# Kernel optimization log

Hardware: AMD Instinct MI355X
Metric: run time of the kernel (lower is better)

The kernel has to match this reference:

```python
import jax, jax.numpy as jnp
import numpy as np
from jax import lax

B, C, H, W = 2, 64, 48, 48
NH, DK, DV = 8, 64, 128          # heads, per-head d_k, per-head d_v
DN, NS, R = 128, 16, 4           # SS2D d_inner (expand=2), d_state, dt_rank
MULT = 4                          # FFN expansion
L = H * W


def layer_norm(x, w, b, eps=1e-5):
    m = x.mean(-1, keepdims=True)
    v = ((x - m) ** 2).mean(-1, keepdims=True)
    return (x - m) / jnp.sqrt(v + eps) * w + b


def conv2d(x, w, groups=1):
    # x: NCHW, w: OIHW
    return lax.conv_general_dilated(x, w, (1, 1), 'SAME',
                                    dimension_numbers=('NCHW', 'OIHW', 'NCHW'),
                                    feature_group_count=groups)


def setup_inputs() -> dict:
    key = jax.random.key(0)
    ks = jax.random.split(key, 24)
    rn = lambda k, shp, s=0.02: jax.random.normal(k, shp, jnp.float32) * s
    inp = {
        'enc_input': jax.random.normal(ks[0], (B, C, H, W), jnp.float32),
        'slf_attn_snr': jax.random.uniform(ks[1], (B, 1, H, W), jnp.float32),
        # MultiHeadAttention params
        'attn_wq': rn(ks[2], (C, NH * DK)),
        'attn_wk': rn(ks[3], (C, NH * DK)),
        'attn_wv': rn(ks[4], (C, NH * DV)),
        'attn_fc': rn(ks[5], (NH * DV, C)),
        'attn_ln_w': jnp.ones((C,), jnp.float32),
        'attn_ln_b': jnp.zeros((C,), jnp.float32),
        # SS2D params
        'ss_in_w': rn(ks[6], (C, 2 * DN)),
        'ss_conv_w': rn(ks[7], (DN, 1, 3, 3)),
        'ss_conv_b': jnp.zeros((DN,), jnp.float32),
        'ss_xproj_w': rn(ks[8], (4, R + 2 * NS, DN)),
        'ss_dt_w': rn(ks[9], (4, DN, R)),
        'ss_dt_b': rn(ks[10], (4, DN)),
        'ss_Alog': jnp.log(jnp.broadcast_to(jnp.arange(1, NS + 1, dtype=jnp.float32), (4, DN, NS))),
        'ss_D': jnp.ones((4, DN), jnp.float32),
        'ss_norm_w': jnp.ones((DN,), jnp.float32),
        'ss_norm_b': jnp.zeros((DN,), jnp.float32),
        'ss_out_w': rn(ks[11], (DN, C)),
        # FFN (PreNorm + conv block)
        'ffn_ln_w': jnp.ones((C,), jnp.float32),
        'ffn_ln_b': jnp.zeros((C,), jnp.float32),
        'ffn_w1': rn(ks[12], (C * MULT, C, 1, 1)),
        'ffn_dw': rn(ks[13], (C * MULT, 1, 3, 3)),
        'ffn_w2': rn(ks[14], (C, C * MULT, 1, 1)),
    }
    return inp


def reference(enc_input, slf_attn_snr, attn_wq, attn_wk, attn_wv, attn_fc,
              attn_ln_w, attn_ln_b, ss_in_w, ss_conv_w, ss_conv_b, ss_xproj_w,
              ss_dt_w, ss_dt_b, ss_Alog, ss_D, ss_norm_w, ss_norm_b, ss_out_w,
              ffn_ln_w, ffn_ln_b, ffn_w1, ffn_dw, ffn_w2):
    # ---- Multi-head self-attention over spatial tokens (SNR-biased) ----
    x_tok = enc_input.reshape(B, C, L).transpose(0, 2, 1)        # (B, L, C)
    q = (x_tok @ attn_wq).reshape(B, L, NH, DK).transpose(0, 2, 1, 3)
    k = (x_tok @ attn_wk).reshape(B, L, NH, DK).transpose(0, 2, 1, 3)
    v = (x_tok @ attn_wv).reshape(B, L, NH, DV).transpose(0, 2, 1, 3)
    scores = jnp.einsum('bhqd,bhkd->bhqk', q, k) / jnp.sqrt(jnp.float32(DK))
    snr_flat = slf_attn_snr.reshape(B, 1, 1, L)                  # bias over keys
    scores = scores + jnp.log(snr_flat + 1e-4)
    attn = jax.nn.softmax(scores, axis=-1)                       # (B, NH, L, L)
    o = jnp.einsum('bhqk,bhkd->bhqd', attn, v)
    o = o.transpose(0, 2, 1, 3).reshape(B, L, NH * DV) @ attn_fc
    enc_output = layer_norm(o + x_tok, attn_ln_w, attn_ln_b)     # post-LN residual
    enc_output = enc_output.transpose(0, 2, 1).reshape(B, C, H, W)

    # ---- SS2D: 4-direction 2D selective scan ----
    xh = enc_output.transpose(0, 2, 3, 1)                        # (B, H, W, C)
    snr_h = slf_attn_snr.transpose(0, 2, 3, 1)                   # (B, H, W, 1)
    xz = xh @ ss_in_w                                            # (B, H, W, 2*DN)
    x1, z = xz[..., :DN], xz[..., DN:]
    x1 = x1.transpose(0, 3, 1, 2)                                # (B, DN, H, W)
    x1 = conv2d(x1, ss_conv_w, groups=DN) + ss_conv_b[None, :, None, None]
    x1 = jax.nn.silu(x1)

    x_hw = x1.reshape(B, DN, L)
    x_wh = x1.transpose(0, 1, 3, 2).reshape(B, DN, L)
    xs = jnp.stack([x_hw, x_wh], axis=1)                         # (B, 2, DN, L)
    xs = jnp.concatenate([xs, jnp.flip(xs, axis=-1)], axis=1)    # (B, 4, DN, L)

    x_dbl = jnp.einsum('bkdl,kcd->bkcl', xs, ss_xproj_w)
    dts, Bs, Cs = x_dbl[:, :, :R], x_dbl[:, :, R:R + NS], x_dbl[:, :, R + NS:]
    dts = jnp.einsum('bkrl,kdr->bkdl', dts, ss_dt_w) + ss_dt_b[None, :, :, None]
    dts = jax.nn.softplus(dts)                                   # (B, 4, DN, L)
    A = -jnp.exp(ss_Alog)                                        # (4, DN, NS)

    def step(h, inp):
        xt, dtt, Bt, Ct = inp                                    # (B,4,DN),(B,4,DN),(B,4,NS),(B,4,NS)
        dA = jnp.exp(dtt[..., None] * A)                         # (B,4,DN,NS)
        h = h * dA + (dtt * xt)[..., None] * Bt[:, :, None, :]
        y = jnp.einsum('bkdn,bkn->bkd', h, Ct)
        return h, y

    h0 = jnp.zeros((B, 4, DN, NS), jnp.float32)
    elems = (xs.transpose(3, 0, 1, 2), dts.transpose(3, 0, 1, 2),
             Bs.transpose(3, 0, 1, 2), Cs.transpose(3, 0, 1, 2))
    _, ys = lax.scan(step, h0, elems)                            # (L, B, 4, DN)
    ys = ys.transpose(1, 2, 3, 0) + ss_D[None, :, :, None] * xs  # (B, 4, DN, L)

    inv = jnp.flip(ys[:, 2:4], axis=-1)                          # undo reversed scans
    wh = ys[:, 1].reshape(B, DN, W, H).transpose(0, 1, 3, 2).reshape(B, DN, L)
    invwh = inv[:, 1].reshape(B, DN, W, H).transpose(0, 1, 3, 2).reshape(B, DN, L)
    y = ys[:, 0] + inv[:, 0] + wh + invwh                        # (B, DN, L)
    y = y.transpose(0, 2, 1).reshape(B, H, W, DN)
    y = layer_norm(y, ss_norm_w, ss_norm_b) * jax.nn.silu(z) * snr_h
    x2 = y @ ss_out_w + enc_input.transpose(0, 2, 3, 1)          # (B, H, W, C)

    # ---- PreNorm conv FeedForward ----
    xn = layer_norm(x2, ffn_ln_w, ffn_ln_b).transpose(0, 3, 1, 2)
    h1 = jax.nn.gelu(conv2d(xn, ffn_w1), approximate=False)
    h1 = jax.nn.gelu(conv2d(h1, ffn_dw, groups=C * MULT), approximate=False)
    h1 = conv2d(h1, ffn_w2).transpose(0, 2, 3, 1)
    x3 = h1 + x2

    return x3.transpose(0, 3, 1, 2)                              # (B, C, H, W)
```

## Files before the change

### kernel.cpp

```cpp
#include <hip/hip_runtime.h>
#include <hip/hip_bf16.h>

#define Bq 2
#define Cc 64
#define Hh 48
#define Ww 48
#define Ll 2304
#define NHh 8
#define DKk 64
#define DVv 128
#define DNn 128
#define NSs 16
#define Rr 4
#define SCH 48
#define SNC 48
#define TT 8

#define OQ    0u
#define OK_   2359296u
#define OV    4718592u
#define OO    9437184u
#define OLP   14450688u
#define OX2   15040512u
#define OVT   15630336u
#define WS_NEED_FLOATS (OVT + 4718592u)
#define ODT2  OQ
#define OYS2  OK_
#define OX1P  OV
#define OZ    (OV + 589824u)
#define OX1S  (OV + 1179648u)
#define OBS2  (OV + 1769472u)
#define OCS2  (OV + 2064384u)
#define OCSA  (OV + 2359296u)
#define OCSB  (OV + 3145728u)
#define OHST  (OV + 3932160u)
#define OH1A  OO
#define OH1B  (OO + 1179648u)

typedef short short8v __attribute__((ext_vector_type(8)));
typedef short short4v __attribute__((ext_vector_type(4)));
typedef float f32x4 __attribute__((ext_vector_type(4)));
typedef unsigned short ushort_t;

__device__ __forceinline__ float geluf(float x) {
  return 0.5f * x * (1.0f + erff(x * 0.70710678118654752f));
}
__device__ __forceinline__ float siluf(float x) {
  return x / (1.0f + __expf(-x));
}
__device__ __forceinline__ float softplusf(float x) {
  return fmaxf(x, 0.0f) + log1pf(__expf(-fabsf(x)));
}
__device__ __forceinline__ int spmap(int k, int l) {
  if (k == 0) return l;
  if (k == 1) return (l % 48) * 48 + l / 48;
  if (k == 2) return 2303 - l;
  int l2 = 2303 - l; return (l2 % 48) * 48 + l2 / 48;
}
__device__ __forceinline__ short f2bf(float f) {
  unsigned u = __float_as_uint(f);
  unsigned r = (u + 0x7FFFu + ((u >> 16) & 1u)) >> 16;
  return (short)r;
}

__global__ void k_code(float* out) { if (threadIdx.x == 0) out[0] = 25000.f; }

__global__ __launch_bounds__(256) void k_qkv(const float* __restrict__ enc,
    const float* __restrict__ wq, const float* __restrict__ wk,
    const float* __restrict__ wv, float* __restrict__ ws) {
  int l0 = blockIdx.x * TT; int b = blockIdx.y;
  int t = threadIdx.x;
  __shared__ float xs[64][12];
  {
    int idx = t, c = idx >> 3, i = idx & 7;
    xs[c][i] = enc[(size_t)b * Cc * Ll + (size_t)c * Ll + l0 + i];
    idx = t + 256; c = idx >> 3; i = idx & 7;
    xs[c][i] = enc[(size_t)b * Cc * Ll + (size_t)c * Ll + l0 + i];
  }
  __syncthreads();
  ushort_t* qb = (ushort_t*)(ws + OQ);
  ushort_t* kb = (ushort_t*)(ws + OK_);
  float* v = ws + OV;
#pragma unroll
  for (int g = 0; g < 6; ++g) {
    int j = t + g * 256;
    float acc[TT];
#pragma unroll
    for (int i = 0; i < TT; ++i) acc[i] = 0.f;
    const float* wp; int col, stride;
    if (j < 512) { wp = wq + j; stride = 512; col = j; }
    else if (j < 1024) { wp = wk + (j - 512); stride = 512; col = j - 512; }
    else { wp = wv + (j - 1024); stride = 1024; col = j - 1024; }
    for (int c = 0; c < 64; ++c) {
      float w = wp[(size_t)c * stride];
      const float4* xc = (const float4*)&xs[c][0];
      float4 x0 = xc[0], x1 = xc[1];
      acc[0] += x0.x * w; acc[1] += x0.y * w;
      acc[2] += x0.z * w; acc[3] += x0.w * w;
      acc[4] += x1.x * w; acc[5] += x1.y * w;
      acc[6] += x1.z * w; acc[7] += x1.w * w;
    }
    if (j < 512) {
#pragma unroll
      for (int i = 0; i < TT; ++i)
        qb[((size_t)(b * 8 + (col >> 6)) * Ll + l0 + i) * 64 + (col & 63)] =
            (ushort_t)f2bf(acc[i] * 0.125f);
    } else if (j < 1024) {
#pragma unroll
      for (int i = 0; i < TT; ++i)
        kb[((size_t)(b * 8 + (col >> 6)) * Ll + l0 + i) * 64 + (col & 63)] =
            (ushort_t)f2bf(acc[i]);
    } else {
#pragma unroll
      for (int i = 0; i < TT; ++i)
        v[((size_t)(b * 8 + (col >> 7)) * Ll + l0 + i) * 128 + (col & 127)] = acc[i];
    }
  }
}

__global__ __launch_bounds__(256) void k_vt(float* __restrict__ ws) {
  int bh = blockIdx.y;
  int l0 = blockIdx.x * 64;
  int t = threadIdx.x;
  __shared__ float tile[128][65];
  const float* vp = ws + OV + ((size_t)bh * Ll + l0) * 128;
  for (int i = t; i < 64 * 32; i += 256) {
    int l = i >> 5, dv4 = (i & 31) * 4;
    float4 a = *(const float4*)(vp + (size_t)l * 128 + dv4);
    tile[dv4][l] = a.x; tile[dv4 + 1][l] = a.y;
    tile[dv4 + 2][l] = a.z; tile[dv4 + 3][l] = a.w;
  }
  __syncthreads();
  ushort_t* vt = (ushort_t*)(ws + OVT) + (size_t)bh * 128 * Ll + l0;
  for (int i = t; i < 128 * 16; i += 256) {
    int dv = i >> 4, l4 = (i & 15) * 4;
    short4v a;
    a[0] = f2bf(tile[dv][l4]); a[1] = f2bf(tile[dv][l4 + 1]);
    a[2] = f2bf(tile[dv][l4 + 2]); a[3] = f2bf(tile[dv][l4 + 3]);
    *(short4v*)(vt + (size_t)dv * Ll + l4) = a;
  }
}

#define NKT2 18
#define LSK 72
__global__ __launch_bounds__(256) void k_attn(const float* __restrict__ snr,
                                              float* __restrict__ ws) {
  int bh = blockIdx.y; int b = bh >> 3; int hd = bh & 7;
  int q0 = blockIdx.x * 64;
  int ks = blockIdx.z;
  int kbase = ks * (Ll / 2);
  int t = threadIdx.x;
  int w = t >> 6, lane = t & 63;
  int m16 = lane & 15, quad = lane >> 4;

  __shared__ __align__(16) ushort_t Ks[64 * LSK];
  __shared__ __align__(16) ushort_t Vs[128 * LSK];
  __shared__ __align__(16) ushort_t Ps[4 * 16 * LSK];
  __shared__ float sfac_s[64];

  const ushort_t* qbf = (const ushort_t*)(ws + OQ) + (size_t)bh * Ll * 64;
  const ushort_t* kbf = (const ushort_t*)(ws + OK_) + (size_t)bh * Ll * 64;
  const ushort_t* vtb = (const ushort_t*)(ws + OVT) + (size_t)bh * 128 * Ll;

  short8v qa[2];
  {
    const ushort_t* qrp = qbf + (size_t)(q0 + w * 16 + m16) * 64 + quad * 8;
    qa[0] = *(const short8v*)qrp;
    qa[1] = *(const short8v*)(qrp + 32);
  }
  int sk_key = t >> 2, sk_d0 = (t & 3) * 16;
  int sv_dv = t >> 1, sv_k0 = (t & 1) * 32;

  short8v kreg[2], vreg[4];
  float snr_reg = 0.f;
  {
    const ushort_t* ksrc = kbf + (size_t)(kbase + sk_key) * 64 + sk_d0;
    kreg[0] = *(const short8v*)ksrc;
    kreg[1] = *(const short8v*)(ksrc + 8);
    const ushort_t* vsrc = vtb + (size_t)sv_dv * Ll + kbase + sv_k0;
#pragma unroll
    for (int i = 0; i < 4; ++i) vreg[i] = *(const short8v*)(vsrc + i * 8);
    if (t < 64) snr_reg = snr[b * Ll + kbase + t];
  }

  f32x4 oacc[8];
#pragma unroll
  for (int i = 0; i < 8; ++i) oacc[i] = (f32x4)0.f;
  float l_r[4] = {0.f, 0.f, 0.f, 0.f};

  for (int kt = 0; kt < NKT2; ++kt) {
    __syncthreads();
    *(short8v*)&Ks[sk_key * LSK + sk_d0] = kreg[0];
    *(short8v*)&Ks[sk_key * LSK + sk_d0 + 8] = kreg[1];
#pragma unroll
    for (int i = 0; i < 4; ++i)
      *(short8v*)&Vs[sv_dv * LSK + sv_k0 + i * 8] = vreg[i];
    if (t < 64) sfac_s[t] = snr_reg + 1e-4f;
    __syncthreads();
    if (kt + 1 < NKT2) {
      int k0n = kbase + (kt + 1) * 64;
      const ushort_t* ksrc = kbf + (size_t)(k0n + sk_key) * 64 + sk_d0;
      kreg[0] = *(const short8v*)ksrc;
      kreg[1] = *(const short8v*)(ksrc + 8);
      const ushort_t* vsrc = vtb + (size_t)sv_dv * Ll + k0n + sv_k0;
#pragma unroll
      for (int i = 0; i < 4; ++i) vreg[i] = *(const short8v*)(vsrc + i * 8);
      if (t < 64) snr_reg = snr[b * Ll + k0n + t];
    }

    f32x4 sac[4];
#pragma unroll
    for (int n = 0; n < 4; ++n) {
      int key = n * 16 + m16;
      short8v kb0 = *(const short8v*)&Ks[key * LSK + quad * 8];
      short8v kb1 = *(const short8v*)&Ks[key * LSK + 32 + quad * 8];
      f32x4 acc = (f32x4)0.f;
      acc = __builtin_amdgcn_mfma_f32_16x16x32_bf16(qa[0], kb0, acc, 0, 0, 0);
      acc = __builtin_amdgcn_mfma_f32_16x16x32_bf16(qa[1], kb1, acc, 0, 0, 0);
      sac[n] = acc;
    }
    float sf[4];
#pragma unroll
    for (int n = 0; n < 4; ++n) sf[n] = sfac_s[n * 16 + m16];
    ushort_t* pw = &Ps[w * 16 * LSK];
#pragma unroll
    for (int r = 0; r < 4; ++r) {
#pragma unroll
      for (int n = 0; n < 4; ++n) {
        float p = __expf(sac[n][r]) * sf[n];
        l_r[r] += p;
        pw[(quad * 4 + r) * LSK + n * 16 + m16] = (ushort_t)f2bf(p);
      }
    }
    short8v pb0 = *(const short8v*)&pw[m16 * LSK + quad * 8];
    short8v pb1 = *(const short8v*)&pw[m16 * LSK + 32 + quad * 8];
#pragma unroll
    for (int dt_ = 0; dt_ < 8; ++dt_) {
      const ushort_t* vrow = &Vs[(dt_ * 16 + m16) * LSK];
      short8v va0 = *(const short8v*)&vrow[quad * 8];
      short8v va1 = *(const short8v*)&vrow[32 + quad * 8];
      f32x4 o = oacc[dt_];
      o = __builtin_amdgcn_mfma_f32_16x16x32_bf16(va0, pb0, o, 0, 0, 0);
      o = __builtin_amdgcn_mfma_f32_16x16x32_bf16(va1, pb1, o, 0, 0, 0);
      oacc[dt_] = o;
    }
  }
#pragma unroll
  for (int r = 0; r < 4; ++r) {
    float lv = l_r[r];
    lv += __shfl_xor(lv, 1, 64);
    lv += __shfl_xor(lv, 2, 64);
    lv += __shfl_xor(lv, 4, 64);
    lv += __shfl_xor(lv, 8, 64);
    l_r[r] = lv;
  }
  if (m16 == 0) {
    float* lp = ws + OLP + (size_t)ks * (Bq * NHh * Ll) + (size_t)bh * Ll;
#pragma unroll
    for (int r = 0; r < 4; ++r) lp[q0 + w * 16 + quad * 4 + r] = l_r[r];
  }
  float* opb = ws + (ks ? OV : OO);
  float* op = opb + ((size_t)(b * Ll + q0 + w * 16 + m16)) * 1024 + hd * 128;
#pragma unroll
  for (int dt_ = 0; dt_ < 8; ++dt_) {
#pragma unroll
    for (int r = 0; r < 4; ++r) {
      op[dt_ * 16 + quad * 4 + r] = oacc[dt_][r];
    }
  }
}

__global__ __launch_bounds__(256) void k_ocomb(float* __restrict__ ws) {
  size_t e4 = (size_t)blockIdx.x * 256 + threadIdx.x;
  int c4 = (int)(e4 & 255);
  size_t bl = e4 >> 8;
  int b = (int)(bl / Ll), l = (int)(bl % Ll);
  int hd = c4 >> 5;
  int bh = b * 8 + hd;
  float l1 = ws[OLP + (size_t)bh * Ll + l];
  float l2 = ws[OLP + (size_t)(Bq * NHh * Ll) + (size_t)bh * Ll + l];
  float linv = 1.f / (l1 + l2);
  float4* po = (float4*)(ws + OO) + e4;
  const float4* pv = (const float4*)(ws + OV) + e4;
  float4 a = *po, bq = *pv;
  a.x = (a.x + bq.x) * linv;
  a.y = (a.y + bq.y) * linv;
  a.z = (a.z + bq.z) * linv;
  a.w = (a.w + bq.w) * linv;
  *po = a;
}

__global__ __launch_bounds__(256) void k_oprojxz(const float* __restrict__ enc,
    const float* __restrict__ fc, const float* __restrict__ lnw,
    const float* __restrict__ lnb, const float* __restrict__ ssin,
    float* __restrict__ ws) {
  int l0 = blockIdx.x * TT, b = blockIdx.y, t = threadIdx.x;
  __shared__ float orow[1024][9];
  __shared__ float part[4][TT][64];
  __shared__ float xh_s[64][9];
  const float* op = ws + OO + ((size_t)(b * Ll + l0)) * 1024;
#pragma unroll
  for (int k = 0; k < 4; ++k) {
    int c = t + k * 256;
#pragma unroll
    for (int i = 0; i < TT; ++i) orow[c][i] = op[(size_t)i * 1024 + c];
  }
  __syncthreads();
  int col = t & 63, seg = t >> 6;
  {
    float acc[TT];
#pragma unroll
    for (int i = 0; i < TT; ++i) acc[i] = 0.f;
    const float* fcs = fc + (size_t)(seg * 256) * 64 + col;
    for (int c = 0; c < 256; ++c) {
      float w = fcs[(size_t)c * 64];
      const float* orc = &orow[seg * 256 + c][0];
#pragma unroll
      for (int i = 0; i < TT; ++i) acc[i] += orc[i] * w;
    }
#pragma unroll
    for (int i = 0; i < TT; ++i) part[seg][i][col] = acc[i];
  }
  __syncthreads();
  if (t < 64) {
    float lw = lnw[t], lb = lnb[t];
#pragma unroll
    for (int i = 0; i < TT; ++i) {
      float a = part[0][i][t] + part[1][i][t] + part[2][i][t] + part[3][i][t];
      a += enc[(size_t)b * Cc * Ll + (size_t)t * Ll + l0 + i];
      float s = a;
#pragma unroll
      for (int o = 32; o >= 1; o >>= 1) s += __shfl_xor(s, o, 64);
      float m = s * (1.f / 64.f);
      float dd = a - m;
      float vs = dd * dd;
#pragma unroll
      for (int o = 32; o >= 1; o >>= 1) vs += __shfl_xor(vs, o, 64);
      xh_s[t][i] = dd * rsqrtf(vs * (1.f / 64.f) + 1e-5f) * lw + lb;
    }
  }
  __syncthreads();
  {
    float acc2[TT];
#pragma unroll
    for (int i = 0; i < TT; ++i) acc2[i] = 0.f;
    for (int c = 0; c < 64; ++c) {
      float w = ssin[c * 256 + t];
      const float* xc = &xh_s[c][0];
#pragma unroll
      for (int i = 0; i < TT; ++i) acc2[i] += xc[i] * w;
    }
    if (t < 128) {
#pragma unroll
      for (int i = 0; i < TT; ++i)
        ws[OX1P + ((size_t)(b * Ll + l0 + i)) * 128 + t] = acc2[i];
    } else {
#pragma unroll
      for (int i = 0; i < TT; ++i)
        ws[OZ + ((size_t)(b * Ll + l0 + i)) * 128 + (t - 128)] = acc2[i];
    }
  }
}

__global__ __launch_bounds__(256) void k_conv(const float* __restrict__ cw,
    const float* __restrict__ cb, float* __restrict__ ws) {
  int l0 = blockIdx.x * TT, b = blockIdx.y, t = threadIdx.x;
  int h = l0 / 48, w0 = l0 % 48;
  __shared__ float tile[3][10][128];
  for (int idx = t; idx < 3840; idx += 256) {
    int r = idx / 1280, rem = idx % 1280;
    int col = rem >> 7, d = rem & 127;
    int hh = h + r - 1, wx = w0 + col - 1;
    float v = 0.f;
    if (hh >= 0 && hh < 48 && wx >= 0 && wx < 48)
      v = ws[OX1P + ((size_t)(b * Ll + hh * 48 + wx)) * 128 + d];
    tile[r][col][d] = v;
  }
  __syncthreads();
  int d = t & 127, half = t >> 7;
  float cwr[9];
#pragma unroll
  for (int j = 0; j < 9; ++j) cwr[j] = cw[d * 9 + j];
  float cbv = cb[d];
#pragma unroll
  for (int j = 0; j < 4; ++j) {
    int i = half * 4 + j;
    float acc = cbv;
#pragma unroll
    for (int kh = 0; kh < 3; ++kh)
#pragma unroll
      for (int kw = 0; kw < 3; ++kw)
        acc += tile[kh][i + kw][d] * cwr[kh * 3 + kw];
    ws[OX1S + ((size_t)(b * Ll + l0 + i)) * 128 + d] = siluf(acc);
  }
}

__global__ __launch_bounds__(128) void k_xdbl(const float* __restrict__ xw,
    const float* __restrict__ dtw, const float* __restrict__ dtb,
    float* __restrict__ ws) {
  int l0 = blockIdx.x * TT;
  int by = blockIdx.y; int b = by >> 2; int k = by & 3;
  int t = threadIdx.x;
  __shared__ float xv[128][9];
  __shared__ float pr[36][TT];
#pragma unroll
  for (int i = 0; i < TT; ++i) {
    int sp = spmap(k, l0 + i);
    xv[t][i] = ws[OX1S + ((size_t)(b * Ll) + sp) * 128 + t];
  }
  __syncthreads();
  if (t < 36) {
    float s[TT];
#pragma unroll
    for (int i = 0; i < TT; ++i) s[i] = 0.f;
    const float* wp = xw + (size_t)(k * 36 + t) * 128;
    for (int d = 0; d < 128; ++d) {
      float w = wp[d];
      const float* xc = &xv[d][0];
#pragma unroll
      for (int i = 0; i < TT; ++i) s[i] += xc[i] * w;
    }
#pragma unroll
    for (int i = 0; i < TT; ++i) pr[t][i] = s[i];
  }
  __syncthreads();
  {
    int d = t;
    const float* wp = dtw + (size_t)(k * 128 + d) * 4;
    float w0 = wp[0], w1 = wp[1], w2 = wp[2], w3 = wp[3];
    float bb = dtb[k * 128 + d];
#pragma unroll
    for (int i = 0; i < TT; ++i) {
      float v = pr[0][i] * w0 + pr[1][i] * w1 + pr[2][i] * w2 + pr[3][i] * w3 + bb;
      ws[ODT2 + ((size_t)(by * Ll + l0 + i)) * 128 + d] = softplusf(v);
    }
  }
  if (t < 16) {
#pragma unroll
    for (int i = 0; i < TT; ++i)
      ws[OBS2 + ((size_t)(by * Ll + l0 + i)) * 16 + t] = pr[4 + t][i];
  } else if (t < 32) {
#pragma unroll
    for (int i = 0; i < TT; ++i)
      ws[OCS2 + ((size_t)(by * Ll + l0 + i)) * 16 + (t - 16)] = pr[20 + (t - 16)][i];
  }
}

__global__ __launch_bounds__(256) void k_scanA(const float* __restrict__ alog,
                                               float* __restrict__ ws) {
  int c = blockIdx.x;
  int bk = blockIdx.y;
  int b = bk >> 2, k = bk & 3;
  int t = threadIdx.x;
  int n = t & 15, dg = t >> 4;
  __shared__ float dt_s[2][128], x_s[2][128], Bs_s[2][16];
  float A_r[8], ap[8], bc[8];
#pragma unroll
  for (int i = 0; i < 8; ++i) {
    int d = dg * 8 + i;
    A_r[i] = -__expf(alog[(size_t)((k * 128 + d) * 16) + n]);
    ap[i] = 1.f; bc[i] = 0.f;
  }
  const float* dtp = ws + ODT2 + ((size_t)bk * Ll) * 128;
  const float* bsp = ws + OBS2 + ((size_t)bk * Ll) * 16;
  const float* xb = ws + OX1S + (size_t)b * Ll * 128;
  float r_a = 0.f, r_Bs = 0.f;
  {
    int l = c * SCH;
    int sp = spmap(k, l);
    if (t < 128) r_a = dtp[(size_t)l * 128 + t];
    else r_a = xb[(size_t)sp * 128 + (t - 128)];
    if (t < 16) r_Bs = bsp[(size_t)l * 16 + t];
  }
  for (int ll = 0; ll < SCH; ++ll) {
    int buf = ll & 1;
    if (t < 128) dt_s[buf][t] = r_a;
    else x_s[buf][t - 128] = r_a;
    if (t < 16) Bs_s[buf][t] = r_Bs;
    __syncthreads();
    if (ll + 1 < SCH) {
      int l2 = c * SCH + ll + 1;
      int sp2 = spmap(k, l2);
      if (t < 128) r_a = dtp[(size_t)l2 * 128 + t];
      else r_a = xb[(size_t)sp2 * 128 + (t - 128)];
      if (t < 16) r_Bs = bsp[(size_t)l2 * 16 + t];
    }
    float Bv = Bs_s[buf][n];
#pragma unroll
    for (int i = 0; i < 8; ++i) {
      int d = dg * 8 + i;
      float dtv = dt_s[buf][d];
      float a = __expf(dtv * A_r[i]);
      bc[i] = bc[i] * a + dtv * x_s[buf][d] * Bv;
      ap[i] *= a;
    }
  }
  float* csa = ws + OCSA + ((size_t)(bk * SNC + c) * 128) * 16;
  float* csb = ws + OCSB + ((size_t)(bk * SNC + c) * 128) * 16;
#pragma unroll
  for (int i = 0; i < 8; ++i) {
    int d = dg * 8 + i;
    csa[d * 16 + n] = ap[i];
    csb[d * 16 + n] = bc[i];
  }
}

__global__ __launch_bounds__(256) void k_scanB(float* __restrict__ ws) {
  int g = blockIdx.x * 256 + threadIdx.x;
  int bk = g >> 11;
  int dn = g & 2047;
  const float* csa = ws + OCSA;
  const float* csb = ws + OCSB;
  float* hst = ws + OHST;
  size_t base = (size_t)bk * SNC * 2048 + dn;
  float h = 0.f;
  float a = csa[base], bq = csb[base];
  for (int c = 0; c < SNC; ++c) {
    float na = 0.f, nb = 0.f;
    if (c + 1 < SNC) {
      size_t idx2 = base + (size_t)(c + 1) * 2048;
      na = csa[idx2]; nb = csb[idx2];
    }
    hst[base + (size_t)c * 2048] = h;
    h = a * h + bq;
    a = na; bq = nb;
  }
}

__global__ __launch_bounds__(256) void k_scanC(const float* __restrict__ alog,
    const float* __restrict__ Dp, float* __restrict__ ws) {
  int c = blockIdx.x, bk = blockIdx.y;
  int b = bk >> 2, k = bk & 3;
  int t = threadIdx.x;
  int n = t & 15, dg = t >> 4;
  __shared__ float dt_s[2][128], x_s[2][128], Bs_s[2][16], Cs_s[2][16];
  float A_r[8], h[8], Dv[8];
#pragma unroll
  for (int i = 0; i < 8; ++i) {
    int d = dg * 8 + i;
    A_r[i] = -__expf(alog[(size_t)((k * 128 + d) * 16) + n]);
    h[i] = ws[OHST + ((size_t)(bk * SNC + c) * 128 + d) * 16 + n];
    Dv[i] = Dp[k * 128 + d];
  }
  const float* dtp = ws + ODT2 + ((size_t)bk * Ll) * 128;
  const float* bsp = ws + OBS2 + ((size_t)bk * Ll) * 16;
  const float* csp = ws + OCS2 + ((size_t)bk * Ll) * 16;
  const float* xb = ws + OX1S + (size_t)b * Ll * 128;
  float* yp = ws + OYS2 + ((size_t)bk * Ll) * 128;
  float r_a = 0.f, r_bc = 0.f;
  {
    int l = c * SCH;
    int sp = spmap(k, l);
    if (t < 128) r_a = dtp[(size_t)l * 128 + t];
    else r_a = xb[(size_t)sp * 128 + (t - 128)];
    if (t < 16) r_bc = bsp[(size_t)l * 16 + t];
    else if (t < 32) r_bc = csp[(size_t)l * 16 + (t - 16)];
  }
  for (int ll = 0; ll < SCH; ++ll) {
    int buf = ll & 1;
    if (t < 128) dt_s[buf][t] = r_a;
    else x_s[buf][t - 128] = r_a;
    if (t < 16) Bs_s[buf][t] = r_bc;
    else if (t < 32) Cs_s[buf][t - 16] = r_bc;
    __syncthreads();
    if (ll + 1 < SCH) {
      int l2 = c * SCH + ll + 1;
      int sp2 = spmap(k, l2);
      if (t < 128) r_a = dtp[(size_t)l2 * 128 + t];
      else r_a = xb[(size_t)sp2 * 128 + (t - 128)];
      if (t < 16) r_bc = bsp[(size_t)l2 * 16 + t];
      else if (t < 32) r_bc = csp[(size_t)l2 * 16 + (t - 16)];
    }
    int l = c * SCH + ll;
    float Bv = Bs_s[buf][n], Cv = Cs_s[buf][n];
    float yacc[8];
#pragma unroll
    for (int i = 0; i < 8; ++i) {
      int d = dg * 8 + i;
      float dtv = dt_s[buf][d];
      float a = __expf(dtv * A_r[i]);
      h[i] = h[i] * a + dtv * x_s[buf][d] * Bv;
      yacc[i] = h[i] * Cv;
    }
#pragma unroll
    for (int i = 0; i < 8; ++i) {
      float yv = yacc[i];
      yv += __shfl_xor(yv, 1, 64);
      yv += __shfl_xor(yv, 2, 64);
      yv += __shfl_xor(yv, 4, 64);
      yv += __shfl_xor(yv, 8, 64);
      yacc[i] = yv;
    }
    if (n == 0) {
#pragma unroll
      for (int i = 0; i < 8; ++i) {
        int d = dg * 8 + i;
        yp[(size_t)l * 128 + d] = yacc[i] + Dv[i] * x_s[buf][d];
      }
    }
  }
}

__global__ __launch_bounds__(256) void k_combffn1(const float* __restrict__ enc,
    const float* __restrict__ nw, const float* __restrict__ nb,
    const float* __restrict__ snr, const float* __restrict__ ow,
    const float* __restrict__ lw, const float* __restrict__ lb,
    const float* __restrict__ w1, float* __restrict__ ws) {
  int l0 = blockIdx.x * TT, b = blockIdx.y, t = threadIdx.x;
  __shared__ float yr[128][9];
  __shared__ float redm[2][TT], redq[2][TT];
  __shared__ float part[2][TT][64];
  __shared__ float xn_s[64][9];
  int lane = t & 63, wid = (t >> 6) & 1;
  float v[TT], m[TT];
  if (t < 128) {
    int d = t;
    const float* ysb = ws + OYS2;
#pragma unroll
    for (int i = 0; i < TT; ++i) {
      int l = l0 + i;
      int hh = l / 48, wwp = l % 48;
      int lT = wwp * 48 + hh;
      v[i] = ysb[((size_t)(b * 4 + 0) * Ll + l) * 128 + d] +
             ysb[((size_t)(b * 4 + 2) * Ll + (2303 - l)) * 128 + d] +
             ysb[((size_t)(b * 4 + 1) * Ll + lT) * 128 + d] +
             ysb[((size_t)(b * 4 + 3) * Ll + (2303 - lT)) * 128 + d];
    }
    float s[TT];
#pragma unroll
    for (int i = 0; i < TT; ++i) s[i] = v[i];
#pragma unroll
    for (int o = 32; o >= 1; o >>= 1)
#pragma unroll
      for (int i = 0; i < TT; ++i) s[i] += __shfl_xor(s[i], o, 64);
    if (lane == 0) {
#pragma unroll
      for (int i = 0; i < TT; ++i) redm[wid][i] = s[i];
    }
  }
  __syncthreads();
  if (t < 128) {
    float q[TT];
#pragma unroll
    for (int i = 0; i < TT; ++i) {
      m[i] = (redm[0][i] + redm[1][i]) * (1.f / 128.f);
      float dv = v[i] - m[i];
      q[i] = dv * dv;
    }
#pragma unroll
    for (int o = 32; o >= 1; o >>= 1)
#pragma unroll
      for (int i = 0; i < TT; ++i) q[i] += __shfl_xor(q[i], o, 64);
    if (lane == 0) {
#pragma unroll
      for (int i = 0; i < TT; ++i) redq[wid][i] = q[i];
    }
  }
  __syncthreads();
  if (t < 128) {
    int d = t;
    float nwv = nw[d], nbv = nb[d];
#pragma unroll
    for (int i = 0; i < TT; ++i) {
      int l = l0 + i;
      float var = (redq[0][i] + redq[1][i]) * (1.f / 128.f);
      float y = (v[i] - m[i]) * rsqrtf(var + 1e-5f) * nwv + nbv;
      float zv = ws[OZ + ((size_t)(b * Ll + l)) * 128 + d];
      y *= siluf(zv);
      y *= snr[b * Ll + l];
      yr[d][i] = y;
    }
  }
  __syncthreads();
  if (t < 128) {
    int col = t & 63, seg = t >> 6;
    float acc[TT];
#pragma unroll
    for (int i = 0; i < TT; ++i) acc[i] = 0.f;
    const float* ows = ow + (size_t)(seg * 64) * 64 + col;
    for (int c = 0; c < 64; ++c) {
      float w = ows[c * 64];
      const float* yc = &yr[seg * 64 + c][0];
#pragma unroll
      for (int i = 0; i < TT; ++i) acc[i] += yc[i] * w;
    }
#pragma unroll
    for (int i = 0; i < TT; ++i) part[seg][i][col] = acc[i];
  }
  __syncthreads();
  if (t < 64) {
    float lwv = lw[t], lbv = lb[t];
#pragma unroll
    for (int i = 0; i < TT; ++i) {
      float a = part[0][i][t] + part[1][i][t];
      a += enc[(size_t)b * Cc * Ll + (size_t)t * Ll + l0 + i];
      ws[OX2 + ((size_t)(b * Ll + l0 + i)) * 64 + t] = a;
      float s = a;
#pragma unroll
      for (int o = 32; o >= 1; o >>= 1) s += __shfl_xor(s, o, 64);
      float mm = s * (1.f / 64.f);
      float dd2 = a - mm;
      float vs = dd2 * dd2;
#pragma unroll
      for (int o = 32; o >= 1; o >>= 1) vs += __shfl_xor(vs, o, 64);
      xn_s[t][i] = dd2 * rsqrtf(vs * (1.f / 64.f) + 1e-5f) * lwv + lbv;
    }
  }
  __syncthreads();
  {
    float acc2[TT];
#pragma unroll
    for (int i = 0; i < TT; ++i) acc2[i] = 0.f;
    const float* wp = w1 + (size_t)t * 64;
    for (int c = 0; c < 64; ++c) {
      float w = wp[c];
      const float* xc = &xn_s[c][0];
#pragma unroll
      for (int i = 0; i < TT; ++i) acc2[i] += xc[i] * w;
    }
#pragma unroll
    for (int i = 0; i < TT; ++i)
      ws[OH1A + ((size_t)(b * Ll + l0 + i)) * 256 + t] = geluf(acc2[i]);
  }
}

__global__ __launch_bounds__(256) void k_ffndw(const float* __restrict__ dww,
                                               float* __restrict__ ws) {
  int l0 = blockIdx.x * TT, b = blockIdx.y, t = threadIdx.x;
  int h = l0 / 48, w0 = l0 % 48;
  __shared__ float tile[3][10][256];
  for (int idx = t; idx < 7680; idx += 256) {
    int r = idx / 2560, rem = idx % 2560;
    int col = rem >> 8, ch = rem & 255;
    int hh = h + r - 1, wx = w0 + col - 1;
    float v = 0.f;
    if (hh >= 0 && hh < 48 && wx >= 0 && wx < 48)
      v = ws[OH1A + ((size_t)(b * Ll + hh * 48 + wx)) * 256 + ch];
    tile[r][col][ch] = v;
  }
  __syncthreads();
  float dwr[9];
#pragma unroll
  for (int j = 0; j < 9; ++j) dwr[j] = dww[t * 9 + j];
#pragma unroll
  for (int i = 0; i < TT; ++i) {
    float acc = 0.f;
#pragma unroll
    for (int kh = 0; kh < 3; ++kh)
#pragma unroll
      for (int kw = 0; kw < 3; ++kw)
        acc += tile[kh][i + kw][t] * dwr[kh * 3 + kw];
    ws[OH1B + ((size_t)(b * Ll + l0 + i)) * 256 + t] = geluf(acc);
  }
}

__global__ __launch_bounds__(256) void k_ffn2(const float* __restrict__ w2,
                                              float* __restrict__ ws,
                                              float* __restrict__ out) {
  int l0 = blockIdx.x * TT, b = blockIdx.y, t = threadIdx.x;
  __shared__ float hr[256][9];
  __shared__ float part[4][TT][64];
  const float* hp = ws + OH1B + ((size_t)(b * Ll + l0)) * 256;
#pragma unroll
  for (int i = 0; i < TT; ++i) hr[t][i] = hp[(size_t)i * 256 + t];
  __syncthreads();
  int col = t & 63, seg = t >> 6;
  {
    float acc[TT];
#pragma unroll
    for (int i = 0; i < TT; ++i) acc[i] = 0.f;
    const float* wp = w2 + (size_t)col * 256 + seg * 64;
    for (int c = 0; c < 64; ++c) {
      float w = wp[c];
      const float* hc = &hr[seg * 64 + c][0];
#pragma unroll
      for (int i = 0; i < TT; ++i) acc[i] += hc[i] * w;
    }
#pragma unroll
    for (int i = 0; i < TT; ++i) part[seg][i][col] = acc[i];
  }
  __syncthreads();
  if (t < 64) {
    float av[TT];
#pragma unroll
    for (int i = 0; i < TT; ++i) {
      float a = part[0][i][t] + part[1][i][t] + part[2][i][t] + part[3][i][t];
      av[i] = a + ws[OX2 + ((size_t)(b * Ll + l0 + i)) * 64 + t];
    }
    float* opx = out + ((size_t)(b * 64 + t)) * 2304 + l0;
    *(float4*)opx = make_float4(av[0], av[1], av[2], av[3]);
    *((float4*)opx + 1) = make_float4(av[4], av[5], av[6], av[7]);
  }
}

extern "C" void kernel_launch(void* const* d_in, const int* in_sizes, int n_in,
                              void* d_out, int out_size, void* d_ws, size_t ws_size,
                              hipStream_t stream) {
  (void)in_sizes; (void)n_in; (void)out_size;
  const float* enc  = (const float*)d_in[0];
  const float* snr  = (const float*)d_in[1];
  const float* wq   = (const float*)d_in[2];
  const float* wk   = (const float*)d_in[3];
  const float* wv   = (const float*)d_in[4];
  const float* fc   = (const float*)d_in[5];
  const float* alnw = (const float*)d_in[6];
  const float* alnb = (const float*)d_in[7];
  const float* ssin = (const float*)d_in[8];
  const float* cw   = (const float*)d_in[9];
  const float* cb   = (const float*)d_in[10];
  const float* xw   = (const float*)d_in[11];
  const float* dtw  = (const float*)d_in[12];
  const float* dtb  = (const float*)d_in[13];
  const float* alog = (const float*)d_in[14];
  const float* Dp   = (const float*)d_in[15];
  const float* nw   = (const float*)d_in[16];
  const float* nb   = (const float*)d_in[17];
  const float* ow   = (const float*)d_in[18];
  const float* flnw = (const float*)d_in[19];
  const float* flnb = (const float*)d_in[20];
  const float* w1   = (const float*)d_in[21];
  const float* dww  = (const float*)d_in[22];
  const float* w2   = (const float*)d_in[23];
  float* ws = (float*)d_ws;
  float* out = (float*)d_out;

  if (ws_size < (size_t)WS_NEED_FLOATS * 4) {
    hipLaunchKernelGGL(k_code, dim3(1), dim3(64), 0, stream, out);
    return;
  }

  hipLaunchKernelGGL(k_qkv, dim3(Ll / TT, Bq), dim3(256), 0, stream, enc, wq, wk, wv, ws);
  hipLaunchKernelGGL(k_vt, dim3(Ll / 64, Bq * NHh), dim3(256), 0, stream, ws);
  hipLaunchKernelGGL(k_attn, dim3(Ll / 64, Bq * NHh, 2), dim3(256), 0, stream, snr, ws);
  hipLaunchKernelGGL(k_ocomb, dim3(Bq * Ll, 1), dim3(256), 0, stream, ws);
  hipLaunchKernelGGL(k_oprojxz, dim3(Ll / TT, Bq), dim3(256), 0, stream, enc, fc, alnw, alnb, ssin, ws);
  hipLaunchKernelGGL(k_conv, dim3(Ll / TT, Bq), dim3(256), 0, stream, cw, cb, ws);
  hipLaunchKernelGGL(k_xdbl, dim3(Ll / TT, Bq * 4), dim3(128), 0, stream, xw, dtw, dtb, ws);
  hipLaunchKernelGGL(k_scanA, dim3(SNC, Bq * 4), dim3(256), 0, stream, alog, ws);
  hipLaunchKernelGGL(k_scanB, dim3(64), dim3(256), 0, stream, ws);
  hipLaunchKernelGGL(k_scanC, dim3(SNC, Bq * 4), dim3(256), 0, stream, alog, Dp, ws);
  hipLaunchKernelGGL(k_combffn1, dim3(Ll / TT, Bq), dim3(256), 0, stream, enc, nw, nb, snr, ow, flnw, flnb, w1, ws);
  hipLaunchKernelGGL(k_ffndw, dim3(Ll / TT, Bq), dim3(256), 0, stream, dww, ws);
  hipLaunchKernelGGL(k_ffn2, dim3(Ll / TT, Bq), dim3(256), 0, stream, w2, ws, out);
}
```

Measured before the change: 433.7 us.

## Fuse split-K attention output combine into output projection kernel

Removes the separate k_ocomb kernel. k_oprojxz now reads both split-K partial outputs and the two softmax denominators, then combines and normalises them while loading into shared memory. This saves one launch plus a full read-modify-write pass over the 1024-wide attention output. The workspace layout is reshuffled so X1P, Z, LP and X2 no longer alias buffers that are still live. Separately, the LayerNorm stages in two kernels now spread over all four wavefronts instead of only the first 64 threads.

```diff
diff --git a/kernel.cpp b/kernel.cpp
--- a/kernel.cpp
+++ b/kernel.cpp
@@ -20,14 +20,14 @@
 #define OK_   2359296u
 #define OV    4718592u
 #define OO    9437184u
-#define OLP   14450688u
-#define OX2   15040512u
+#define OX1P  14450688u
+#define OZ    15040512u
 #define OVT   15630336u
+#define OLP   (OVT + 2359296u)
+#define OX2   0u
 #define WS_NEED_FLOATS (OVT + 4718592u)
 #define ODT2  OQ
 #define OYS2  OK_
-#define OX1P  OV
-#define OZ    (OV + 589824u)
 #define OX1S  (OV + 1179648u)
 #define OBS2  (OV + 1769472u)
 #define OCS2  (OV + 2064384u)
@@ -270,26 +270,6 @@
   }
 }
 
-__global__ __launch_bounds__(256) void k_ocomb(float* __restrict__ ws) {
-  size_t e4 = (size_t)blockIdx.x * 256 + threadIdx.x;
-  int c4 = (int)(e4 & 255);
-  size_t bl = e4 >> 8;
-  int b = (int)(bl / Ll), l = (int)(bl % Ll);
-  int hd = c4 >> 5;
-  int bh = b * 8 + hd;
-  float l1 = ws[OLP + (size_t)bh * Ll + l];
-  float l2 = ws[OLP + (size_t)(Bq * NHh * Ll) + (size_t)bh * Ll + l];
-  float linv = 1.f / (l1 + l2);
-  float4* po = (float4*)(ws + OO) + e4;
-  const float4* pv = (const float4*)(ws + OV) + e4;
-  float4 a = *po, bq = *pv;
-  a.x = (a.x + bq.x) * linv;
-  a.y = (a.y + bq.y) * linv;
-  a.z = (a.z + bq.z) * linv;
-  a.w = (a.w + bq.w) * linv;
-  *po = a;
-}
-
 __global__ __launch_bounds__(256) void k_oprojxz(const float* __restrict__ enc,
     const float* __restrict__ fc, const float* __restrict__ lnw,
     const float* __restrict__ lnb, const float* __restrict__ ssin,
@@ -298,12 +278,25 @@
   __shared__ float orow[1024][9];
   __shared__ float part[4][TT][64];
   __shared__ float xh_s[64][9];
-  const float* op = ws + OO + ((size_t)(b * Ll + l0)) * 1024;
+  __shared__ float linv_s[8][TT];
+  if (t < 64) {
+    int hd = t >> 3, i = t & 7;
+    float l1 = ws[OLP + (size_t)(b * 8 + hd) * Ll + l0 + i];
+    float l2 = ws[OLP + (size_t)(Bq * NHh * Ll) + (size_t)(b * 8 + hd) * Ll + l0 + i];
+    linv_s[hd][i] = 1.f / (l1 + l2);
+  }
+  __syncthreads();
+  const float* op0 = ws + OO + ((size_t)(b * Ll + l0)) * 1024;
+  const float* op1 = ws + OV + ((size_t)(b * Ll + l0)) * 1024;
 #pragma unroll
   for (int k = 0; k < 4; ++k) {
     int c = t + k * 256;
-#pragma unroll
-    for (int i = 0; i < TT; ++i) orow[c][i] = op[(size_t)i * 1024 + c];
+    float li[TT];
+#pragma unroll
+    for (int i = 0; i < TT; ++i) li[i] = linv_s[c >> 7][i];
+#pragma unroll
+    for (int i = 0; i < TT; ++i)
+      orow[c][i] = (op0[(size_t)i * 1024 + c] + op1[(size_t)i * 1024 + c]) * li[i];
   }
   __syncthreads();
   int col = t & 63, seg = t >> 6;
@@ -322,12 +315,13 @@
     for (int i = 0; i < TT; ++i) part[seg][i][col] = acc[i];
   }
   __syncthreads();
-  if (t < 64) {
-    float lw = lnw[t], lb = lnb[t];
-#pragma unroll
-    for (int i = 0; i < TT; ++i) {
-      float a = part[0][i][t] + part[1][i][t] + part[2][i][t] + part[3][i][t];
-      a += enc[(size_t)b * Cc * Ll + (size_t)t * Ll + l0 + i];
+  {
+    float lw = lnw[col], lb = lnb[col];
+#pragma unroll
+    for (int i2 = 0; i2 < 2; ++i2) {
+      int i = seg * 2 + i2;
+      float a = part[0][i][col] + part[1][i][col] + part[2][i][col] + part[3][i][col];
+      a += enc[(size_t)b * Cc * Ll + (size_t)col * Ll + l0 + i];
       float s = a;
 #pragma unroll
       for (int o = 32; o >= 1; o >>= 1) s += __shfl_xor(s, o, 64);
@@ -336,7 +330,7 @@
       float vs = dd * dd;
 #pragma unroll
       for (int o = 32; o >= 1; o >>= 1) vs += __shfl_xor(vs, o, 64);
-      xh_s[t][i] = dd * rsqrtf(vs * (1.f / 64.f) + 1e-5f) * lw + lb;
+      xh_s[col][i] = dd * rsqrtf(vs * (1.f / 64.f) + 1e-5f) * lw + lb;
     }
   }
   __syncthreads();
@@ -688,13 +682,15 @@
     for (int i = 0; i < TT; ++i) part[seg][i][col] = acc[i];
   }
   __syncthreads();
-  if (t < 64) {
-    float lwv = lw[t], lbv = lb[t];
-#pragma unroll
-    for (int i = 0; i < TT; ++i) {
-      float a = part[0][i][t] + part[1][i][t];
-      a += enc[(size_t)b * Cc * Ll + (size_t)t * Ll + l0 + i];
-      ws[OX2 + ((size_t)(b * Ll + l0 + i)) * 64 + t] = a;
+  {
+    int wv = t >> 6, col2 = t & 63;
+    float lwv = lw[col2], lbv = lb[col2];
+#pragma unroll
+    for (int i2 = 0; i2 < 2; ++i2) {
+      int i = wv * 2 + i2;
+      float a = part[0][i][col2] + part[1][i][col2];
+      a += enc[(size_t)b * Cc * Ll + (size_t)col2 * Ll + l0 + i];
+      ws[OX2 + ((size_t)(b * Ll + l0 + i)) * 64 + col2] = a;
       float s = a;
 #pragma unroll
       for (int o = 32; o >= 1; o >>= 1) s += __shfl_xor(s, o, 64);
@@ -703,7 +699,7 @@
       float vs = dd2 * dd2;
 #pragma unroll
       for (int o = 32; o >= 1; o >>= 1) vs += __shfl_xor(vs, o, 64);
-      xn_s[t][i] = dd2 * rsqrtf(vs * (1.f / 64.f) + 1e-5f) * lwv + lbv;
+      xn_s[col2][i] = dd2 * rsqrtf(vs * (1.f / 64.f) + 1e-5f) * lwv + lbv;
     }
   }
   __syncthreads();
@@ -832,7 +828,6 @@
   hipLaunchKernelGGL(k_qkv, dim3(Ll / TT, Bq), dim3(256), 0, stream, enc, wq, wk, wv, ws);
   hipLaunchKernelGGL(k_vt, dim3(Ll / 64, Bq * NHh), dim3(256), 0, stream, ws);
   hipLaunchKernelGGL(k_attn, dim3(Ll / 64, Bq * NHh, 2), dim3(256), 0, stream, snr, ws);
-  hipLaunchKernelGGL(k_ocomb, dim3(Bq * Ll, 1), dim3(256), 0, stream, ws);
   hipLaunchKernelGGL(k_oprojxz, dim3(Ll / TT, Bq), dim3(256), 0, stream, enc, fc, alnw, alnb, ssin, ws);
   hipLaunchKernelGGL(k_conv, dim3(Ll / TT, Bq), dim3(256), 0, stream, cw, cb, ws);
   hipLaunchKernelGGL(k_xdbl, dim3(Ll / TT, Bq * 4), dim3(128), 0, stream, xw, dtw, dtb, ws);
```

Measured after the change: 424.7 us. -2.1%, faster.
